# Performance work log

Measured on AMD Instinct MI355X. Metric: run time of the kernel, lower is better.

The kernel has to match this reference:

```python
import jax, jax.numpy as jnp
import numpy as np

N_EMBD = 1024
N_HEAD = 16
HEAD_DIM = N_EMBD // N_HEAD
BLOCK = 2048
BATCH = 2


def setup_inputs() -> dict:
    key = jax.random.key(0)
    ks = jax.random.split(key, 6)
    s_in = 1.0 / np.sqrt(N_EMBD)
    s_hd = 1.0 / np.sqrt(N_EMBD)  # fan-in of c_proj1 is n_head*head_dim = n_embd
    return {
        "x": jax.random.normal(ks[0], (BATCH, BLOCK, N_EMBD), jnp.float32),
        "wq": jax.random.normal(ks[1], (N_EMBD, N_HEAD, HEAD_DIM), jnp.float32) * s_in,
        "wk": jax.random.normal(ks[2], (N_EMBD, N_HEAD, HEAD_DIM), jnp.float32) * s_in,
        "wv": jax.random.normal(ks[3], (N_EMBD, N_HEAD, HEAD_DIM), jnp.float32) * s_in,
        "wp1": jax.random.normal(ks[4], (N_HEAD, HEAD_DIM, N_EMBD), jnp.float32) * s_hd,
        "wp2": jax.random.normal(ks[5], (N_EMBD, N_EMBD), jnp.float32) * s_in,
    }


def reference(x, wq, wk, wv, wp1, wp2):
    # QKV projections: DenseGeneral(features=(H, D), axis=-1), no bias
    q = jnp.einsum('btc,chd->bthd', x, wq)
    k = jnp.einsum('btc,chd->bthd', x, wk)
    v = jnp.einsum('btc,chd->bthd', x, wv)
    scale = HEAD_DIM ** (-0.5)
    wei = jnp.einsum('bqhd,bkhd->bhqk', q, k) * scale  # [B,H,T,T]
    tril = jnp.tril(jnp.ones((BLOCK, BLOCK), dtype=bool))
    wei = jnp.where(tril, wei, -jnp.inf)
    wei = jax.nn.softmax(wei, axis=-1)
    att = jnp.einsum('bhqk,bkhd->bqhd', wei, v)  # [B,T,H,D]
    # c_proj1: DenseGeneral over (-2,-1) -> contract (H,D)
    y = jnp.einsum('bqhd,hdc->bqc', att, wp1)
    # c_proj2: Dense
    out = jnp.einsum('bqc,ce->bqe', y, wp2)
    return out
```

## Files before the change

kernel.cpp:

```cpp
#include <hip/hip_runtime.h>
#include <hip/hip_bf16.h>
#include <stdint.h>

typedef __bf16 bf16;
typedef __bf16 bf16x4 __attribute__((ext_vector_type(4)));
typedef __bf16 bf16x8 __attribute__((ext_vector_type(8)));
typedef float  f32x4  __attribute__((ext_vector_type(4)));

#define MFMA16(a,b,c) __builtin_amdgcn_mfma_f32_16x16x32_bf16((a),(b),(c),0,0,0)

#define TSEQ 2048
#define NE   1024
#define NE3  3072
#define NH   16
#define HD   64
#define MTOK 4096

#if defined(__has_builtin) && __has_builtin(__builtin_amdgcn_exp2f)
#define EXP2F(x) __builtin_amdgcn_exp2f(x)
#else
__device__ __forceinline__ float exp2_fast(float x) {
  float r; asm("v_exp_f32 %0, %1" : "=v"(r) : "v"(x)); return r;
}
#define EXP2F(x) exp2_fast(x)
#endif

__device__ __forceinline__ void gl_lds16(const bf16* g, bf16* l) {
  __builtin_amdgcn_global_load_lds(
      (const __attribute__((address_space(1))) void*)g,
      (__attribute__((address_space(3))) void*)l,
      16, 0, 0);
}

__global__ void k_cast(const float* __restrict__ in, bf16* __restrict__ out, int n4) {
  int i = blockIdx.x * blockDim.x + threadIdx.x;
  if (i < n4) {
    float4 v = reinterpret_cast<const float4*>(in)[i];
    bf16x4 o = { (bf16)v.x, (bf16)v.y, (bf16)v.z, (bf16)v.w };
    reinterpret_cast<bf16x4*>(out)[i] = o;
  }
}

__global__ void k_transpose_all(const float* __restrict__ wq, const float* __restrict__ wk,
                                const float* __restrict__ wv, const float* __restrict__ wp2,
                                const float* __restrict__ wp1,
                                bf16* __restrict__ W3T, bf16* __restrict__ Wp2T,
                                bf16* __restrict__ Wp1b) {
  __shared__ float tile[64][65];
  const int z = blockIdx.z;
  const int r0 = blockIdx.y * 64, c0 = blockIdx.x * 64;
  const int lc = threadIdx.x & 63, lr0 = threadIdx.x >> 6;
  if (z == 4) {
#pragma unroll
    for (int i = 0; i < 16; ++i) {
      int lr = i*4 + lr0;
      Wp1b[(size_t)(r0 + lr)*1024 + c0 + lc] = (bf16)wp1[(size_t)(r0 + lr)*1024 + c0 + lc];
    }
    return;
  }
  const float* in = (z == 0) ? wq : (z == 1) ? wk : (z == 2) ? wv : wp2;
  bf16* out = (z < 3) ? (W3T + (size_t)z * 1024 * 1024) : Wp2T;
#pragma unroll
  for (int i = 0; i < 16; ++i) {
    int lr = i*4 + lr0;
    tile[lr][lc] = in[(size_t)(r0 + lr) * 1024 + (c0 + lc)];
  }
  __syncthreads();
#pragma unroll
  for (int i = 0; i < 16; ++i) {
    int lr = i*4 + lr0;
    out[(size_t)(c0 + lr) * 1024 + (r0 + lc)] = (bf16)tile[lc][lr];
  }
}

template<int BN, typename OutT, bool VTF>
__global__ __launch_bounds__(256) void k_gemm_bt(const bf16* __restrict__ A,
                                                 const bf16* __restrict__ Bt,
                                                 OutT* __restrict__ C,
                                                 bf16* __restrict__ VtOut,
                                                 const int M, const int N, const int K) {
  constexpr int NC = BN / 32;
  __shared__ bf16 As[2][128*32];
  __shared__ bf16 Bs[2][BN*32];
  const int tid  = threadIdx.x;
  const int lane = tid & 63;
  const int wave = tid >> 6;
  const int wr = (wave >> 1) * 64;
  const int wc = (wave & 1) * (BN/2);
  const int l15 = lane & 15;
  const int l4  = lane >> 4;

  const int nwg = gridDim.x * gridDim.y;
  int id = blockIdx.y * gridDim.x + blockIdx.x;
  id = (id & 7) * (nwg >> 3) + (id >> 3);
  const int bm = (id / gridDim.x) * 128;
  const int bn = (id % gridDim.x) * BN;

  const int srow = tid >> 2;
  const int scol = ((tid & 3) ^ ((tid >> 3) & 3)) * 8;
  const bf16* ag = A  + (size_t)(bm + srow) * K + scol;
  const bf16* bg = Bt + (size_t)(bn + srow) * K + scol;
  const int kx = (l4 ^ ((l15 >> 1) & 3)) * 8;

  f32x4 acc[4][NC] = {};

  auto stage = [&](int buf, int k0) {
    bf16* al = As[buf] + tid * 8;
    bf16* bl = Bs[buf] + tid * 8;
    gl_lds16(ag + k0,                   al);
    gl_lds16(ag + k0 + (size_t)64 * K,  al + 64*32);
    gl_lds16(bg + k0,                   bl);
    if (BN == 128) gl_lds16(bg + k0 + (size_t)64 * K, bl + 64*32);
  };

  stage(0, 0);
  __syncthreads();
  int cur = 0;
  for (int k0 = 0; k0 < K; k0 += 32) {
    if (k0 + 32 < K) stage(cur ^ 1, k0 + 32);
    bf16x8 af[4], bfr[NC];
#pragma unroll
    for (int m = 0; m < 4; ++m)
      af[m] = *reinterpret_cast<const bf16x8*>(&As[cur][(wr + m*16 + l15)*32 + kx]);
#pragma unroll
    for (int n = 0; n < NC; ++n)
      bfr[n] = *reinterpret_cast<const bf16x8*>(&Bs[cur][(wc + n*16 + l15)*32 + kx]);
#pragma unroll
    for (int m = 0; m < 4; ++m)
#pragma unroll
      for (int n = 0; n < NC; ++n)
        acc[m][n] = MFMA16(af[m], bfr[n], acc[m][n]);
    __syncthreads();
    cur ^= 1;
  }

  if (VTF && bn >= 2048) {
    const int bB  = bm >> 11;
    const int tb0 = (bm & 2047) + wr + l4*4;
#pragma unroll
    for (int m = 0; m < 4; ++m) {
      const int tb = tb0 + m*16;
#pragma unroll
      for (int n = 0; n < NC; ++n) {
        const int dg = (bn - 2048) + wc + n*16 + l15;
        bf16x4 ov;
#pragma unroll
        for (int r = 0; r < 4; ++r) ov[r] = (bf16)acc[m][n][r];
        *reinterpret_cast<bf16x4*>(
            &VtOut[((size_t)(bB*16 + (dg >> 6))*64 + (dg & 63))*2048 + tb]) = ov;
      }
    }
  } else {
#pragma unroll
    for (int m = 0; m < 4; ++m) {
      const int row = bm + wr + m*16 + l4*4;
#pragma unroll
      for (int n = 0; n < NC; ++n) {
        const int col = bn + wc + n*16 + l15;
#pragma unroll
        for (int r = 0; r < 4; ++r)
          C[(size_t)(row + r) * N + col] = (OutT)acc[m][n][r];
      }
    }
  }
}

__global__ __launch_bounds__(512) void k_attn(const bf16* __restrict__ QKV,
                                              const bf16* __restrict__ Vt,
                                              bf16* __restrict__ O) {
  __shared__ bf16 Ks[2][2*128*32];
  __shared__ bf16 Vs[2][4*64*32];
  __shared__ bf16 Ps[8][4*16*32];

  const int tid  = threadIdx.x;
  const int lane = tid & 63;
  const int wave = tid >> 6;
  const int l15 = lane & 15;
  const int l4  = lane >> 4;

  const int x  = blockIdx.x;
  const int p  = x >> 5;
  const int bh = x & 31;
  const int b  = bh >> 4, h = bh & 15;

  const bf16* Qb = QKV + (size_t)b*TSEQ*NE3 +        h*HD;
  const bf16* Kb = QKV + (size_t)b*TSEQ*NE3 + 1024 + h*HD;
  const bf16* Vb = Vt  + (size_t)bh*HD*TSEQ;
  bf16* Pw = Ps[wave];

  const float SC = 0.125f * 1.44269504f;
  const int swz = (l4 ^ ((l15 >> 1) & 3)) * 8;
  const int key = (l15 >> 1) & 3;

  const int krow = tid >> 2;
  const int kg   = (tid & 3) ^ ((krow >> 1) & 3);
  const int vd   = (tid >> 2) & 63;
  const int vg   = (tid & 3) ^ ((vd >> 1) & 3);
  const int vp0  = tid >> 8;

  auto stage = [&](int buf, int t) {
#pragma unroll
    for (int kk = 0; kk < 2; ++kk)
      gl_lds16(&Kb[(size_t)(t*128 + krow)*NE3 + kk*32 + kg*8],
               &Ks[buf][kk*4096 + tid*8]);
#pragma unroll
    for (int kk = 0; kk < 2; ++kk) {
      const int ksv = kk*2 + vp0;
      gl_lds16(&Vb[(size_t)vd*TSEQ + t*128 + ksv*32 + vg*8],
               &Vs[buf][kk*4096 + tid*8]);
    }
  };

  stage(0, 0);
  __syncthreads();
  int cur = 0;
  int i = 0;

  for (int ci = 0; ci < 2; ++ci) {
    const int c  = ci ? (15 - p) : p;
    const int qw = c*128 + wave*16;

    bf16x8 qf[2];
#pragma unroll
    for (int ks = 0; ks < 2; ++ks) {
      bf16x8 qv = *reinterpret_cast<const bf16x8*>(
          &Qb[(size_t)(qw + l15)*NE3 + ks*32 + l4*8]);
#pragma unroll
      for (int j = 0; j < 8; ++j) qv[j] = (bf16)((float)qv[j] * SC);
      qf[ks] = qv;
    }

    f32x4 ot[4] = {};
    float m_run = -1e30f;
    float l_part = 0.f;

    for (int t = 0; t <= c; ++t, ++i) {
      if (i + 1 < 17) {
        const int nxt = (i + 1 <= p) ? (i + 1) : (i - p);
        stage(cur ^ 1, nxt);
      }

      __builtin_amdgcn_s_setprio(1);
      f32x4 st[8];
#pragma unroll
      for (int kvf = 0; kvf < 8; ++kvf) {
        st[kvf] = f32x4{0.f, 0.f, 0.f, 0.f};
        const int row = kvf*16 + l15;
#pragma unroll
        for (int ks = 0; ks < 2; ++ks) {
          bf16x8 kf = *reinterpret_cast<const bf16x8*>(&Ks[cur][ks*4096 + row*32 + swz]);
          st[kvf] = MFMA16(kf, qf[ks], st[kvf]);
        }
      }
      __builtin_amdgcn_s_setprio(0);

      if (t == c) {
#pragma unroll
        for (int kvf = 0; kvf < 8; ++kvf)
#pragma unroll
          for (int r = 0; r < 4; ++r)
            if (kvf*16 + l4*4 + r > wave*16 + l15) st[kvf][r] = -1e30f;
      }

      float mx = st[0][0];
#pragma unroll
      for (int kvf = 0; kvf < 8; ++kvf)
#pragma unroll
        for (int r = 0; r < 4; ++r) mx = fmaxf(mx, st[kvf][r]);
      mx = fmaxf(mx, __shfl_xor(mx, 16));
      mx = fmaxf(mx, __shfl_xor(mx, 32));

      if (__any(mx > m_run + 8.f)) {
        const float mnew = fmaxf(m_run, mx);
        const float corr = EXP2F(m_run - mnew);
        l_part *= corr;
#pragma unroll
        for (int n2 = 0; n2 < 4; ++n2) ot[n2] *= corr;
        m_run = mnew;
      }

      float rs = 0.f;
#pragma unroll
      for (int kvf = 0; kvf < 8; ++kvf) {
        bf16x4 pk;
#pragma unroll
        for (int r = 0; r < 4; ++r) {
          const float pv = EXP2F(st[kvf][r] - m_run);
          rs += pv;
          pk[r] = (bf16)pv;
        }
        const int gp = (((kvf & 1)*2 + (l4 >> 1)) ^ key);
        *reinterpret_cast<bf16x4*>(
            &Pw[(kvf>>1)*512 + l15*32 + gp*8 + (l4 & 1)*4]) = pk;
      }
      l_part += rs;

      bf16x8 pa[4];
#pragma unroll
      for (int ksv = 0; ksv < 4; ++ksv)
        pa[ksv] = *reinterpret_cast<const bf16x8*>(&Pw[ksv*512 + l15*32 + swz]);
      __builtin_amdgcn_s_setprio(1);
#pragma unroll
      for (int n2 = 0; n2 < 4; ++n2) {
        const int vrow = n2*16 + l15;
#pragma unroll
        for (int ksv = 0; ksv < 4; ++ksv) {
          bf16x8 vf = *reinterpret_cast<const bf16x8*>(&Vs[cur][ksv*2048 + vrow*32 + swz]);
          ot[n2] = MFMA16(vf, pa[ksv], ot[n2]);
        }
      }
      __builtin_amdgcn_s_setprio(0);

      __syncthreads();
      cur ^= 1;
    }

    float l = l_part;
    l += __shfl_xor(l, 16);
    l += __shfl_xor(l, 32);
    const float rl = 1.f / l;
    const size_t row = (size_t)(b*TSEQ + qw + l15);
#pragma unroll
    for (int n2 = 0; n2 < 4; ++n2) {
      bf16x4 ov;
#pragma unroll
      for (int r = 0; r < 4; ++r) ov[r] = (bf16)(ot[n2][r] * rl);
      *reinterpret_cast<bf16x4*>(&O[row*NE + h*HD + n2*16 + l4*4]) = ov;
    }
  }
}

extern "C" void kernel_launch(void* const* d_in, const int* in_sizes, int n_in,
                              void* d_out, int out_size, void* d_ws, size_t ws_size,
                              hipStream_t stream) {
  const float* x   = (const float*)d_in[0];
  const float* wq  = (const float*)d_in[1];
  const float* wk  = (const float*)d_in[2];
  const float* wv  = (const float*)d_in[3];
  const float* wp1 = (const float*)d_in[4];
  const float* wp2 = (const float*)d_in[5];
  float* out = (float*)d_out;

  char* ws = (char*)d_ws;
  const size_t MB = 1024ull * 1024ull;
  bf16* xb   = (bf16*)(ws + 0*MB);
  bf16* W3T  = (bf16*)(ws + 8*MB);
  bf16* wp1b = (bf16*)(ws + 14*MB);
  bf16* wp2T = (bf16*)(ws + 16*MB);
  bf16* WcT  = (bf16*)(ws + 18*MB);
  bf16* QKVb = (bf16*)(ws + 20*MB);
  bf16* Vtb  = (bf16*)(ws + 44*MB);
  bf16* attb = (bf16*)(ws + 52*MB);

  k_cast<<<4096, 256, 0, stream>>>(x, xb, MTOK*NE/4);
  k_transpose_all<<<dim3(16, 16, 5), 256, 0, stream>>>(wq, wk, wv, wp2, wp1,
                                                       W3T, wp2T, wp1b);

  k_gemm_bt<64, bf16, false><<<dim3(16, 8), 256, 0, stream>>>(
      wp2T, wp1b, WcT, nullptr, 1024, 1024, 1024);

  k_gemm_bt<128, bf16, true><<<dim3(24, 32), 256, 0, stream>>>(
      xb, W3T, QKVb, Vtb, MTOK, NE3, NE);

  k_attn<<<dim3(256), 512, 0, stream>>>(QKVb, Vtb, attb);

  k_gemm_bt<128, float, false><<<dim3(8, 32), 256, 0, stream>>>(
      attb, WcT, out, nullptr, MTOK, NE, NE);
}
```

Before: 125.4 us.

## Merge prep kernels and QKV/Wc GEMMs into single launches, narrow output GEMM tile

Folds the x cast and the weight transposes into one prep launch, and runs the Wc = wp2T·wp1 GEMM as extra blocks inside the QKV GEMM launch, cutting two kernel launches and their tail gaps. The output projection now uses 64-wide column tiles with 512 blocks, giving more parallelism across CUs. It also removes the s_setprio hints around the MFMA sections in attention. The Wc GEMM now uses 128-wide tiles with only 64 blocks appended to the grid, so its load balance may differ.

```diff
diff --git a/kernel.cpp b/kernel.cpp
--- a/kernel.cpp
+++ b/kernel.cpp
@@ -32,23 +32,29 @@
       16, 0, 0);
 }
 
-__global__ void k_cast(const float* __restrict__ in, bf16* __restrict__ out, int n4) {
-  int i = blockIdx.x * blockDim.x + threadIdx.x;
-  if (i < n4) {
-    float4 v = reinterpret_cast<const float4*>(in)[i];
+__global__ __launch_bounds__(256) void k_prep(const float* __restrict__ x,
+                                              const float* __restrict__ wq,
+                                              const float* __restrict__ wk,
+                                              const float* __restrict__ wv,
+                                              const float* __restrict__ wp2,
+                                              const float* __restrict__ wp1,
+                                              bf16* __restrict__ xb,
+                                              bf16* __restrict__ W3T,
+                                              bf16* __restrict__ Wp2T,
+                                              bf16* __restrict__ Wp1b) {
+  const int id = blockIdx.x;
+  if (id < 4096) {
+    const int i = id * 256 + threadIdx.x;
+    float4 v = reinterpret_cast<const float4*>(x)[i];
     bf16x4 o = { (bf16)v.x, (bf16)v.y, (bf16)v.z, (bf16)v.w };
-    reinterpret_cast<bf16x4*>(out)[i] = o;
-  }
-}
-
-__global__ void k_transpose_all(const float* __restrict__ wq, const float* __restrict__ wk,
-                                const float* __restrict__ wv, const float* __restrict__ wp2,
-                                const float* __restrict__ wp1,
-                                bf16* __restrict__ W3T, bf16* __restrict__ Wp2T,
-                                bf16* __restrict__ Wp1b) {
+    reinterpret_cast<bf16x4*>(xb)[i] = o;
+    return;
+  }
   __shared__ float tile[64][65];
-  const int z = blockIdx.z;
-  const int r0 = blockIdx.y * 64, c0 = blockIdx.x * 64;
+  const int wid = id - 4096;
+  const int z  = wid >> 8;
+  const int by = (wid >> 4) & 15, bx = wid & 15;
+  const int r0 = by * 64, c0 = bx * 64;
   const int lc = threadIdx.x & 63, lr0 = threadIdx.x >> 6;
   if (z == 4) {
 #pragma unroll
@@ -73,20 +79,117 @@
   }
 }
 
-template<int BN, typename OutT, bool VTF>
-__global__ __launch_bounds__(256) void k_gemm_bt(const bf16* __restrict__ A,
-                                                 const bf16* __restrict__ Bt,
-                                                 OutT* __restrict__ C,
-                                                 bf16* __restrict__ VtOut,
-                                                 const int M, const int N, const int K) {
-  constexpr int NC = BN / 32;
+__global__ __launch_bounds__(256) void k_gemm_qkv_wc(const bf16* __restrict__ xb,
+                                                     const bf16* __restrict__ W3T,
+                                                     const bf16* __restrict__ wp2T,
+                                                     const bf16* __restrict__ wp1b,
+                                                     bf16* __restrict__ QKV,
+                                                     bf16* __restrict__ Vt,
+                                                     bf16* __restrict__ WcT) {
+  constexpr int K = 1024;
+  __shared__ bf16 As[2][128*32];
+  __shared__ bf16 Bs[2][128*32];
+  const int tid  = threadIdx.x;
+  const int lane = tid & 63;
+  const int wave = tid >> 6;
+  const int wr = (wave >> 1) * 64;
+  const int wc = (wave & 1) * 64;
+  const int l15 = lane & 15;
+  const int l4  = lane >> 4;
+
+  const bf16 *A, *Bt; bf16 *C; int N, nbx; bool vtf;
+  int id = blockIdx.x;
+  if (id < 768) {
+    A = xb; Bt = W3T; C = QKV; N = 3072; nbx = 24; vtf = true;
+    id = (id & 7) * 96 + (id >> 3);
+  } else {
+    id -= 768;
+    A = wp2T; Bt = wp1b; C = WcT; N = 1024; nbx = 8; vtf = false;
+    id = (id & 7) * 8 + (id >> 3);
+  }
+  const int bm = (id / nbx) * 128;
+  const int bn = (id % nbx) * 128;
+
+  const int srow = tid >> 2;
+  const int scol = ((tid & 3) ^ ((tid >> 3) & 3)) * 8;
+  const bf16* ag = A  + (size_t)(bm + srow) * K + scol;
+  const bf16* bg = Bt + (size_t)(bn + srow) * K + scol;
+  const int kx = (l4 ^ ((l15 >> 1) & 3)) * 8;
+
+  f32x4 acc[4][4] = {};
+
+  auto stage = [&](int buf, int k0) {
+    bf16* al = As[buf] + tid * 8;
+    bf16* bl = Bs[buf] + tid * 8;
+    gl_lds16(ag + k0,                  al);
+    gl_lds16(ag + k0 + (size_t)64 * K, al + 64*32);
+    gl_lds16(bg + k0,                  bl);
+    gl_lds16(bg + k0 + (size_t)64 * K, bl + 64*32);
+  };
+
+  stage(0, 0);
+  __syncthreads();
+  int cur = 0;
+  for (int k0 = 0; k0 < K; k0 += 32) {
+    if (k0 + 32 < K) stage(cur ^ 1, k0 + 32);
+    bf16x8 af[4], bfr[4];
+#pragma unroll
+    for (int m = 0; m < 4; ++m)
+      af[m] = *reinterpret_cast<const bf16x8*>(&As[cur][(wr + m*16 + l15)*32 + kx]);
+#pragma unroll
+    for (int n = 0; n < 4; ++n)
+      bfr[n] = *reinterpret_cast<const bf16x8*>(&Bs[cur][(wc + n*16 + l15)*32 + kx]);
+#pragma unroll
+    for (int m = 0; m < 4; ++m)
+#pragma unroll
+      for (int n = 0; n < 4; ++n)
+        acc[m][n] = MFMA16(af[m], bfr[n], acc[m][n]);
+    __syncthreads();
+    cur ^= 1;
+  }
+
+  if (vtf && bn >= 2048) {
+    const int bB  = bm >> 11;
+    const int tb0 = (bm & 2047) + wr + l4*4;
+#pragma unroll
+    for (int m = 0; m < 4; ++m) {
+      const int tb = tb0 + m*16;
+#pragma unroll
+      for (int n = 0; n < 4; ++n) {
+        const int dg = (bn - 2048) + wc + n*16 + l15;
+        bf16x4 ov;
+#pragma unroll
+        for (int r = 0; r < 4; ++r) ov[r] = (bf16)acc[m][n][r];
+        *reinterpret_cast<bf16x4*>(
+            &Vt[((size_t)(bB*16 + (dg >> 6))*64 + (dg & 63))*2048 + tb]) = ov;
+      }
+    }
+  } else {
+#pragma unroll
+    for (int m = 0; m < 4; ++m) {
+      const int row = bm + wr + m*16 + l4*4;
+#pragma unroll
+      for (int n = 0; n < 4; ++n) {
+        const int col = bn + wc + n*16 + l15;
+#pragma unroll
+        for (int r = 0; r < 4; ++r)
+          C[(size_t)(row + r) * N + col] = (bf16)acc[m][n][r];
+      }
+    }
+  }
+}
+
+__global__ __launch_bounds__(256) void k_gemm_out(const bf16* __restrict__ A,
+                                                  const bf16* __restrict__ Bt,
+                                                  float* __restrict__ C) {
+  constexpr int K = 1024, N = 1024, BN = 64;
   __shared__ bf16 As[2][128*32];
   __shared__ bf16 Bs[2][BN*32];
   const int tid  = threadIdx.x;
   const int lane = tid & 63;
   const int wave = tid >> 6;
   const int wr = (wave >> 1) * 64;
-  const int wc = (wave & 1) * (BN/2);
+  const int wc = (wave & 1) * 32;
   const int l15 = lane & 15;
   const int l4  = lane >> 4;
 
@@ -102,15 +205,14 @@
   const bf16* bg = Bt + (size_t)(bn + srow) * K + scol;
   const int kx = (l4 ^ ((l15 >> 1) & 3)) * 8;
 
-  f32x4 acc[4][NC] = {};
+  f32x4 acc[4][2] = {};
 
   auto stage = [&](int buf, int k0) {
     bf16* al = As[buf] + tid * 8;
     bf16* bl = Bs[buf] + tid * 8;
-    gl_lds16(ag + k0,                   al);
-    gl_lds16(ag + k0 + (size_t)64 * K,  al + 64*32);
-    gl_lds16(bg + k0,                   bl);
-    if (BN == 128) gl_lds16(bg + k0 + (size_t)64 * K, bl + 64*32);
+    gl_lds16(ag + k0,                  al);
+    gl_lds16(ag + k0 + (size_t)64 * K, al + 64*32);
+    gl_lds16(bg + k0,                  bl);
   };
 
   stage(0, 0);
@@ -118,49 +220,31 @@
   int cur = 0;
   for (int k0 = 0; k0 < K; k0 += 32) {
     if (k0 + 32 < K) stage(cur ^ 1, k0 + 32);
-    bf16x8 af[4], bfr[NC];
+    bf16x8 af[4], bfr[2];
 #pragma unroll
     for (int m = 0; m < 4; ++m)
       af[m] = *reinterpret_cast<const bf16x8*>(&As[cur][(wr + m*16 + l15)*32 + kx]);
 #pragma unroll
-    for (int n = 0; n < NC; ++n)
+    for (int n = 0; n < 2; ++n)
       bfr[n] = *reinterpret_cast<const bf16x8*>(&Bs[cur][(wc + n*16 + l15)*32 + kx]);
 #pragma unroll
     for (int m = 0; m < 4; ++m)
 #pragma unroll
-      for (int n = 0; n < NC; ++n)
+      for (int n = 0; n < 2; ++n)
         acc[m][n] = MFMA16(af[m], bfr[n], acc[m][n]);
     __syncthreads();
     cur ^= 1;
   }
 
-  if (VTF && bn >= 2048) {
-    const int bB  = bm >> 11;
-    const int tb0 = (bm & 2047) + wr + l4*4;
-#pragma unroll
-    for (int m = 0; m < 4; ++m) {
-      const int tb = tb0 + m*16;
-#pragma unroll
-      for (int n = 0; n < NC; ++n) {
-        const int dg = (bn - 2048) + wc + n*16 + l15;
-        bf16x4 ov;
-#pragma unroll
-        for (int r = 0; r < 4; ++r) ov[r] = (bf16)acc[m][n][r];
-        *reinterpret_cast<bf16x4*>(
-            &VtOut[((size_t)(bB*16 + (dg >> 6))*64 + (dg & 63))*2048 + tb]) = ov;
-      }
-    }
-  } else {
-#pragma unroll
-    for (int m = 0; m < 4; ++m) {
-      const int row = bm + wr + m*16 + l4*4;
-#pragma unroll
-      for (int n = 0; n < NC; ++n) {
-        const int col = bn + wc + n*16 + l15;
-#pragma unroll
-        for (int r = 0; r < 4; ++r)
-          C[(size_t)(row + r) * N + col] = (OutT)acc[m][n][r];
-      }
+#pragma unroll
+  for (int m = 0; m < 4; ++m) {
+    const int row = bm + wr + m*16 + l4*4;
+#pragma unroll
+    for (int n = 0; n < 2; ++n) {
+      const int col = bn + wc + n*16 + l15;
+#pragma unroll
+      for (int r = 0; r < 4; ++r)
+        C[(size_t)(row + r) * N + col] = acc[m][n][r];
     }
   }
 }
@@ -240,7 +324,6 @@
         stage(cur ^ 1, nxt);
       }
 
-      __builtin_amdgcn_s_setprio(1);
       f32x4 st[8];
 #pragma unroll
       for (int kvf = 0; kvf < 8; ++kvf) {
@@ -252,7 +335,6 @@
           st[kvf] = MFMA16(kf, qf[ks], st[kvf]);
         }
       }
-      __builtin_amdgcn_s_setprio(0);
 
       if (t == c) {
 #pragma unroll
@@ -299,7 +381,6 @@
 #pragma unroll
       for (int ksv = 0; ksv < 4; ++ksv)
         pa[ksv] = *reinterpret_cast<const bf16x8*>(&Pw[ksv*512 + l15*32 + swz]);
-      __builtin_amdgcn_s_setprio(1);
 #pragma unroll
       for (int n2 = 0; n2 < 4; ++n2) {
         const int vrow = n2*16 + l15;
@@ -309,7 +390,6 @@
           ot[n2] = MFMA16(vf, pa[ksv], ot[n2]);
         }
       }
-      __builtin_amdgcn_s_setprio(0);
 
       __syncthreads();
       cur ^= 1;
@@ -352,18 +432,11 @@
   bf16* Vtb  = (bf16*)(ws + 44*MB);
   bf16* attb = (bf16*)(ws + 52*MB);
 
-  k_cast<<<4096, 256, 0, stream>>>(x, xb, MTOK*NE/4);
-  k_transpose_all<<<dim3(16, 16, 5), 256, 0, stream>>>(wq, wk, wv, wp2, wp1,
-                                                       W3T, wp2T, wp1b);
-
-  k_gemm_bt<64, bf16, false><<<dim3(16, 8), 256, 0, stream>>>(
-      wp2T, wp1b, WcT, nullptr, 1024, 1024, 1024);
-
-  k_gemm_bt<128, bf16, true><<<dim3(24, 32), 256, 0, stream>>>(
-      xb, W3T, QKVb, Vtb, MTOK, NE3, NE);
+  k_prep<<<5376, 256, 0, stream>>>(x, wq, wk, wv, wp2, wp1, xb, W3T, wp2T, wp1b);
+
+  k_gemm_qkv_wc<<<832, 256, 0, stream>>>(xb, W3T, wp2T, wp1b, QKVb, Vtb, WcT);
 
   k_attn<<<dim3(256), 512, 0, stream>>>(QKVb, Vtb, attb);
 
-  k_gemm_bt<128, float, false><<<dim3(8, 32), 256, 0, stream>>>(
-      attb, WcT, out, nullptr, MTOK, NE, NE);
-}
+  k_gemm_out<<<dim3(16, 32), 256, 0, stream>>>(attb, WcT, out);
+}
```

Result: no change. 123.9 us (-1.1%).
